# Kernel optimization log

Hardware: AMD Instinct MI355X
Metric: run time of the kernel (lower is better)

## Reference

```python
import jax, jax.numpy as jnp
import numpy as np

DEPTH = 2
NW = 4          # number of wires (qubits), fixed by 2x2 patches
NP = 14 * 14    # patches per image
NUM_CLASSES = 10


def _ry(theta):
    c = jnp.cos(theta / 2).astype(jnp.complex64)
    s = jnp.sin(theta / 2).astype(jnp.complex64)
    return jnp.stack([jnp.stack([c, -s], -1), jnp.stack([s, c], -1)], -2)


def _rx(theta):
    c = jnp.cos(theta / 2).astype(jnp.complex64)
    s = (-1j) * jnp.sin(theta / 2).astype(jnp.complex64)
    return jnp.stack([jnp.stack([c, s], -1), jnp.stack([s, c], -1)], -2)


def _rz(theta):
    em = jnp.exp(-0.5j * theta.astype(jnp.complex64))
    ep = jnp.exp(0.5j * theta.astype(jnp.complex64))
    z = jnp.zeros_like(em)
    return jnp.stack([jnp.stack([em, z], -1), jnp.stack([z, ep], -1)], -2)


def _apply1(state, mat, wire):
    # state: (N,2,2,2,2); mat: (2,2) shared or (N,2,2) per-patch
    s = jnp.moveaxis(state, 1 + wire, -1)
    if mat.ndim == 2:
        s = jnp.einsum('...i,ji->...j', s, mat)
    else:
        s = jnp.einsum('n...i,nji->n...j', s, mat)
    return jnp.moveaxis(s, -1, 1 + wire)


def _cnot(state, c, t):
    a0 = jnp.take(state, 0, axis=1 + c)
    a1 = jnp.take(state, 1, axis=1 + c)
    t_ax = 1 + t - (1 if t > c else 0)   # target axis index after control removed
    a1 = jnp.flip(a1, axis=t_ax)
    return jnp.stack([a0, a1], axis=1 + c)


def _circuit(angles, params):
    # angles: (N,4) RY-encoded patch pixels; params: (DEPTH,NW,3)
    N = angles.shape[0]
    state = jnp.zeros((N, 16), jnp.complex64).at[:, 0].set(1.0).reshape(N, 2, 2, 2, 2)
    for w in range(NW):
        state = _apply1(state, _ry(angles[:, w]), w)
    for d in range(DEPTH):
        for w in range(NW):
            state = _apply1(state, _rx(params[d, w, 0]), w)
            state = _apply1(state, _ry(params[d, w, 1]), w)
            state = _apply1(state, _rz(params[d, w, 2]), w)
        for w in range(NW - 1):
            state = _cnot(state, w, w + 1)
        state = _cnot(state, NW - 1, 0)
    probs = state.real ** 2 + state.imag ** 2   # (N,2,2,2,2)
    feats = []
    for w in range(NW):
        p = jnp.moveaxis(probs, 1 + w, 1).reshape(N, 2, 8)
        feats.append(p[:, 0].sum(-1) - p[:, 1].sum(-1))  # <Z_w>
    return jnp.stack(feats, -1)                  # (N,4)


def setup_inputs() -> dict:
    key = jax.random.key(0)
    k1, k2, k3 = jax.random.split(key, 3)
    B = 4096
    x = jax.random.uniform(k1, (B, 1, 28, 28), jnp.float32)
    params = jax.random.normal(k2, (DEPTH, NW, 3), jnp.float32)
    W = jax.random.normal(k3, (NUM_CLASSES, NW * NP), jnp.float32) * 0.02
    b = jnp.zeros((NUM_CLASSES,), jnp.float32)
    return {"x": x, "params": params, "W": W, "b": b}


def reference(x, params, W, b):
    B = x.shape[0]
    # extract all 196 2x2 patches, row-major within each patch (matches view(bsz,-1))
    patches = x[:, 0].reshape(B, 14, 2, 14, 2).transpose(0, 1, 3, 2, 4).reshape(B * NP, 4)
    feats = _circuit(patches, params).reshape(B, NP * NW)  # (B,784)
    logits = feats @ W.T + b
    return jax.nn.log_softmax(logits, axis=-1)
```

## Files before the change

### kernel.cpp

```cpp
#include <hip/hip_runtime.h>
#include <hip/hip_bf16.h>

#define NPATCH 196

__global__ __launch_bounds__(256) void quanv_setup(const float* __restrict__ P,
                                                   float* __restrict__ C) {
  __shared__ float Sr[2][16][16], Si[2][16][16];
  __shared__ float gc[24], gs[24];
  __shared__ float A[4][16][16];
  __shared__ float B0[4][3][8][8];
  __shared__ float B1[4][3][3][4][4];
  __shared__ float B2[4][3][3][3][2][2];
  const int tid = threadIdx.x;
  const int row = tid >> 4, col = tid & 15;

  if (tid < 24) {
    float s, c;
    __sincosf(0.5f * P[tid], &s, &c);
    gc[tid] = c; gs[tid] = s;
  }
  Sr[0][row][col] = (row == col) ? 1.0f : 0.0f;
  Si[0][row][col] = 0.0f;
  __syncthreads();

  int cur = 0;
  for (int d = 0; d < 2; ++d) {
    for (int w = 0; w < 4; ++w) {
      const int m = 8 >> w;
      const int par = row ^ m;
      for (int g = 0; g < 3; ++g) {
        const int gi = (d * 4 + w) * 3 + g;
        const float c = gc[gi], s = gs[gi];
        const float r0 = Sr[cur][row][col], i0 = Si[cur][row][col];
        const float r1 = Sr[cur][par][col], i1 = Si[cur][par][col];
        float rn, in_;
        if (g == 0) {
          rn = c * r0 + s * i1;
          in_ = c * i0 - s * r1;
        } else if (g == 1) {
          const float sg = (row & m) ? s : -s;
          rn = c * r0 + sg * r1;
          in_ = c * i0 + sg * i1;
        } else {
          const float sg = (row & m) ? s : -s;
          rn = c * r0 - sg * i0;
          in_ = c * i0 + sg * r0;
        }
        Sr[cur ^ 1][row][col] = rn;
        Si[cur ^ 1][row][col] = in_;
        cur ^= 1;
        __syncthreads();
      }
    }
    int k = row;
    k ^= (k & 1) ? 8 : 0;
    k ^= (k & 2) ? 1 : 0;
    k ^= (k & 4) ? 2 : 0;
    k ^= (k & 8) ? 4 : 0;
    const float pr = Sr[cur][k][col], pi = Si[cur][k][col];
    Sr[cur ^ 1][row][col] = pr;
    Si[cur ^ 1][row][col] = pi;
    cur ^= 1;
    __syncthreads();
  }

  {
    const int i = row, j = col;
    float s0 = 0, s1 = 0, s2 = 0, s3 = 0;
#pragma unroll
    for (int k = 0; k < 16; ++k) {
      const float pr = Sr[cur][k][i] * Sr[cur][k][j] + Si[cur][k][i] * Si[cur][k][j];
      s0 += (k & 8) ? -pr : pr;
      s1 += (k & 4) ? -pr : pr;
      s2 += (k & 2) ? -pr : pr;
      s3 += (k & 1) ? -pr : pr;
    }
    A[0][i][j] = s0; A[1][i][j] = s1; A[2][i][j] = s2; A[3][i][j] = s3;
  }
  __syncthreads();

  {
    const int w = tid >> 6, ip = (tid >> 3) & 7, jp = tid & 7;
    const float a00 = A[w][ip][jp],     a11 = A[w][ip + 8][jp + 8];
    const float a01 = A[w][ip][jp + 8], a10 = A[w][ip + 8][jp];
    B0[w][0][ip][jp] = 0.5f * (a00 + a11);
    B0[w][1][ip][jp] = 0.5f * (a00 - a11);
    B0[w][2][ip][jp] = 0.5f * (a01 + a10);
  }
  __syncthreads();
  if (tid < 192) {
    const int w = tid / 48, a0 = (tid / 16) % 3, ii = (tid >> 2) & 3, jj = tid & 3;
    const float a00 = B0[w][a0][ii][jj],     a11 = B0[w][a0][ii + 4][jj + 4];
    const float a01 = B0[w][a0][ii][jj + 4], a10 = B0[w][a0][ii + 4][jj];
    B1[w][a0][0][ii][jj] = 0.5f * (a00 + a11);
    B1[w][a0][1][ii][jj] = 0.5f * (a00 - a11);
    B1[w][a0][2][ii][jj] = 0.5f * (a01 + a10);
  }
  __syncthreads();
  if (tid < 144) {
    const int w = tid / 36, a0 = (tid / 12) % 3, a1 = (tid / 4) % 3;
    const int i3 = (tid >> 1) & 1, j3 = tid & 1;
    const float a00 = B1[w][a0][a1][i3][j3],     a11 = B1[w][a0][a1][i3 + 2][j3 + 2];
    const float a01 = B1[w][a0][a1][i3][j3 + 2], a10 = B1[w][a0][a1][i3 + 2][j3];
    B2[w][a0][a1][0][i3][j3] = 0.5f * (a00 + a11);
    B2[w][a0][a1][1][i3][j3] = 0.5f * (a00 - a11);
    B2[w][a0][a1][2][i3][j3] = 0.5f * (a01 + a10);
  }
  __syncthreads();
  if (tid < 108) {
    const int w = tid / 27, r = tid % 27;
    const int a0 = r / 9, a1 = (r / 3) % 3, a2 = r % 3;
    const float a00 = B2[w][a0][a1][a2][0][0], a11 = B2[w][a0][a1][a2][1][1];
    const float a01 = B2[w][a0][a1][a2][0][1], a10 = B2[w][a0][a1][a2][1][0];
    const int base = (3 * a0 + a1) * 9 + 3 * a2;
    C[(base + 0) * 4 + w] = 0.5f * (a00 + a11);
    C[(base + 1) * 4 + w] = 0.5f * (a00 - a11);
    C[(base + 2) * 4 + w] = 0.5f * (a01 + a10);
  }
}

__global__ __launch_bounds__(256) void quanv_main(const float* __restrict__ x,
                                                  const float* __restrict__ W,
                                                  const float* __restrict__ bias,
                                                  const float* __restrict__ C,
                                                  float* __restrict__ out) {
  __shared__ float wred[4][10];
  __shared__ float logits[10];
  __shared__ float snorm;
  const int tid = threadIdx.x;
  const int b = blockIdx.x;

  float lg[10];
#pragma unroll
  for (int k = 0; k < 10; ++k) lg[k] = 0.0f;

  if (tid < NPATCH) {
    const int pi = tid / 14, pj = tid - pi * 14;
    const float* px = x + b * 784 + pi * 56 + pj * 2;
    const float2 r0 = *reinterpret_cast<const float2*>(px);
    const float2 r1 = *reinterpret_cast<const float2*>(px + 28);
    float c0, s0, c1, s1, c2, s2, c3, s3;
    __sincosf(r0.x, &s0, &c0);
    __sincosf(r0.y, &s1, &c1);
    __sincosf(r1.x, &s2, &c2);
    __sincosf(r1.y, &s3, &c3);
    float m01[9], m23[9];
    m01[0] = 1.0f; m01[1] = c1;      m01[2] = s1;
    m01[3] = c0;   m01[4] = c0 * c1; m01[5] = c0 * s1;
    m01[6] = s0;   m01[7] = s0 * c1; m01[8] = s0 * s1;
    m23[0] = 1.0f; m23[1] = c3;      m23[2] = s3;
    m23[3] = c2;   m23[4] = c2 * c3; m23[5] = c2 * s3;
    m23[6] = s2;   m23[7] = s2 * c3; m23[8] = s2 * s3;

    float f0 = 0, f1 = 0, f2 = 0, f3 = 0;
    const float4* C4 = reinterpret_cast<const float4*>(C);
#pragma unroll
    for (int a = 0; a < 9; ++a) {
#pragma unroll
      for (int q = 0; q < 9; ++q) {
        const float pr = m01[a] * m23[q];
        const float4 cc = C4[a * 9 + q];
        f0 += cc.x * pr; f1 += cc.y * pr; f2 += cc.z * pr; f3 += cc.w * pr;
      }
    }
    const float* Wp = W + tid * 4;
#pragma unroll
    for (int k = 0; k < 10; ++k) {
      const float4 wv = *reinterpret_cast<const float4*>(Wp + k * 784);
      lg[k] = f0 * wv.x + f1 * wv.y + f2 * wv.z + f3 * wv.w;
    }
  }

#pragma unroll
  for (int k = 0; k < 10; ++k) {
    float v = lg[k];
    v += __shfl_xor(v, 32);
    v += __shfl_xor(v, 16);
    v += __shfl_xor(v, 8);
    v += __shfl_xor(v, 4);
    v += __shfl_xor(v, 2);
    v += __shfl_xor(v, 1);
    lg[k] = v;
  }
  const int lane = tid & 63, wid = tid >> 6;
  if (lane == 0) {
#pragma unroll
    for (int k = 0; k < 10; ++k) wred[wid][k] = lg[k];
  }
  __syncthreads();
  if (tid < 10)
    logits[tid] = wred[0][tid] + wred[1][tid] + wred[2][tid] + wred[3][tid] + bias[tid];
  __syncthreads();
  if (tid == 0) {
    float m = logits[0];
#pragma unroll
    for (int k = 1; k < 10; ++k) m = fmaxf(m, logits[k]);
    float se = 0;
#pragma unroll
    for (int k = 0; k < 10; ++k) se += expf(logits[k] - m);
    snorm = m + logf(se);
  }
  __syncthreads();
  if (tid < 10) out[b * 10 + tid] = logits[tid] - snorm;
}

extern "C" void kernel_launch(void* const* d_in, const int* in_sizes, int n_in,
                              void* d_out, int out_size, void* d_ws, size_t ws_size,
                              hipStream_t stream) {
  const float* x = (const float*)d_in[0];
  const float* P = (const float*)d_in[1];
  const float* W = (const float*)d_in[2];
  const float* bias = (const float*)d_in[3];
  float* out = (float*)d_out;
  float* C = (float*)d_ws;
  const int B = out_size / 10;

  quanv_setup<<<1, 256, 0, stream>>>(P, C);
  quanv_main<<<B, 256, 0, stream>>>(x, W, bias, C, out);
}
```

Before: 27.60 us.

## Fuse rotation gates into unitaries, pack FMAs, restructure logit reduction

In the setup kernel, each wire's RX·RY·RZ gates are combined into one precomputed 2x2 complex unitary, so 24 gate steps become 8 and there are fewer barriers. The final CNOT permutation is no longer a separate pass; it is folded into the index used by the expectation-matrix build. In the main kernel, the 81-term contraction is factorized into an inner sum over q and an outer scale by a, using two-wide float vectors so the compiler can emit packed FMAs. The wave-wide shuffle reduction is replaced by a 4-lane shuffle plus a 49-entry shared-memory sum done serially by 10 threads, which may add latency to the block tail.

```diff
diff --git a/kernel.cpp b/kernel.cpp
--- a/kernel.cpp
+++ b/kernel.cpp
@@ -3,10 +3,13 @@
 
 #define NPATCH 196
 
+typedef float f2 __attribute__((ext_vector_type(2)));
+
 __global__ __launch_bounds__(256) void quanv_setup(const float* __restrict__ P,
                                                    float* __restrict__ C) {
+  __shared__ float gc[24], gs[24];
+  __shared__ float Ur[8][2][2], Ui[8][2][2];
   __shared__ float Sr[2][16][16], Si[2][16][16];
-  __shared__ float gc[24], gs[24];
   __shared__ float A[4][16][16];
   __shared__ float B0[4][3][8][8];
   __shared__ float B1[4][3][3][4][4];
@@ -23,45 +26,53 @@
   Si[0][row][col] = 0.0f;
   __syncthreads();
 
+  if (tid < 8) {
+    const int base = tid * 3;
+    const float c1 = gc[base], s1 = gs[base];
+    const float c2 = gc[base + 1], s2 = gs[base + 1];
+    const float c3 = gc[base + 2], s3 = gs[base + 2];
+    const float m00r = c2 * c1, m00i = s2 * s1;
+    const float m01r = -s2 * c1, m01i = -c2 * s1;
+    const float m10r = s2 * c1, m10i = -c2 * s1;
+    const float m11r = c2 * c1, m11i = -s2 * s1;
+    Ur[tid][0][0] = c3 * m00r + s3 * m00i;  Ui[tid][0][0] = c3 * m00i - s3 * m00r;
+    Ur[tid][0][1] = c3 * m01r + s3 * m01i;  Ui[tid][0][1] = c3 * m01i - s3 * m01r;
+    Ur[tid][1][0] = c3 * m10r - s3 * m10i;  Ui[tid][1][0] = c3 * m10i + s3 * m10r;
+    Ur[tid][1][1] = c3 * m11r - s3 * m11i;  Ui[tid][1][1] = c3 * m11i + s3 * m11r;
+  }
+  __syncthreads();
+
   int cur = 0;
   for (int d = 0; d < 2; ++d) {
     for (int w = 0; w < 4; ++w) {
+      const int gi = d * 4 + w;
       const int m = 8 >> w;
+      const int bit = (row & m) ? 1 : 0;
       const int par = row ^ m;
-      for (int g = 0; g < 3; ++g) {
-        const int gi = (d * 4 + w) * 3 + g;
-        const float c = gc[gi], s = gs[gi];
-        const float r0 = Sr[cur][row][col], i0 = Si[cur][row][col];
-        const float r1 = Sr[cur][par][col], i1 = Si[cur][par][col];
-        float rn, in_;
-        if (g == 0) {
-          rn = c * r0 + s * i1;
-          in_ = c * i0 - s * r1;
-        } else if (g == 1) {
-          const float sg = (row & m) ? s : -s;
-          rn = c * r0 + sg * r1;
-          in_ = c * i0 + sg * i1;
-        } else {
-          const float sg = (row & m) ? s : -s;
-          rn = c * r0 - sg * i0;
-          in_ = c * i0 + sg * r0;
-        }
-        Sr[cur ^ 1][row][col] = rn;
-        Si[cur ^ 1][row][col] = in_;
-        cur ^= 1;
-        __syncthreads();
-      }
-    }
-    int k = row;
-    k ^= (k & 1) ? 8 : 0;
-    k ^= (k & 2) ? 1 : 0;
-    k ^= (k & 4) ? 2 : 0;
-    k ^= (k & 8) ? 4 : 0;
-    const float pr = Sr[cur][k][col], pi = Si[cur][k][col];
-    Sr[cur ^ 1][row][col] = pr;
-    Si[cur ^ 1][row][col] = pi;
-    cur ^= 1;
-    __syncthreads();
+      const int r0 = bit ? par : row, r1 = bit ? row : par;
+      const float a_r = Sr[cur][r0][col], a_i = Si[cur][r0][col];
+      const float b_r = Sr[cur][r1][col], b_i = Si[cur][r1][col];
+      const float u0r = Ur[gi][bit][0], u0i = Ui[gi][bit][0];
+      const float u1r = Ur[gi][bit][1], u1i = Ui[gi][bit][1];
+      const float rn = u0r * a_r - u0i * a_i + u1r * b_r - u1i * b_i;
+      const float in_ = u0r * a_i + u0i * a_r + u1r * b_i + u1i * b_r;
+      Sr[cur ^ 1][row][col] = rn;
+      Si[cur ^ 1][row][col] = in_;
+      cur ^= 1;
+      __syncthreads();
+    }
+    if (d == 0) {
+      int k = row;
+      k ^= (k & 1) ? 8 : 0;
+      k ^= (k & 2) ? 1 : 0;
+      k ^= (k & 4) ? 2 : 0;
+      k ^= (k & 8) ? 4 : 0;
+      const float pr_ = Sr[cur][k][col], pi_ = Si[cur][k][col];
+      Sr[cur ^ 1][row][col] = pr_;
+      Si[cur ^ 1][row][col] = pi_;
+      cur ^= 1;
+      __syncthreads();
+    }
   }
 
   {
@@ -69,7 +80,12 @@
     float s0 = 0, s1 = 0, s2 = 0, s3 = 0;
 #pragma unroll
     for (int k = 0; k < 16; ++k) {
-      const float pr = Sr[cur][k][i] * Sr[cur][k][j] + Si[cur][k][i] * Si[cur][k][j];
+      int gk = k;
+      gk ^= (gk & 1) ? 8 : 0;
+      gk ^= (gk & 2) ? 1 : 0;
+      gk ^= (gk & 4) ? 2 : 0;
+      gk ^= (gk & 8) ? 4 : 0;
+      const float pr = Sr[cur][gk][i] * Sr[cur][gk][j] + Si[cur][gk][i] * Si[cur][gk][j];
       s0 += (k & 8) ? -pr : pr;
       s1 += (k & 4) ? -pr : pr;
       s2 += (k & 2) ? -pr : pr;
@@ -124,7 +140,7 @@
                                                   const float* __restrict__ bias,
                                                   const float* __restrict__ C,
                                                   float* __restrict__ out) {
-  __shared__ float wred[4][10];
+  __shared__ float red2[49][10];
   __shared__ float logits[10];
   __shared__ float snorm;
   const int tid = threadIdx.x;
@@ -144,52 +160,53 @@
     __sincosf(r0.y, &s1, &c1);
     __sincosf(r1.x, &s2, &c2);
     __sincosf(r1.y, &s3, &c3);
-    float m01[9], m23[9];
-    m01[0] = 1.0f; m01[1] = c1;      m01[2] = s1;
-    m01[3] = c0;   m01[4] = c0 * c1; m01[5] = c0 * s1;
-    m01[6] = s0;   m01[7] = s0 * c1; m01[8] = s0 * s1;
-    m23[0] = 1.0f; m23[1] = c3;      m23[2] = s3;
-    m23[3] = c2;   m23[4] = c2 * c3; m23[5] = c2 * s3;
-    m23[6] = s2;   m23[7] = s2 * c3; m23[8] = s2 * s3;
-
-    float f0 = 0, f1 = 0, f2 = 0, f3 = 0;
-    const float4* C4 = reinterpret_cast<const float4*>(C);
+    const float m01s[9] = {1.0f, c1, s1, c0, c0 * c1, c0 * s1, s0, s0 * c1, s0 * s1};
+    const float m23s[9] = {1.0f, c3, s3, c2, c2 * c3, c2 * s3, s2, s2 * c3, s2 * s3};
+    f2 m23b[9];
+#pragma unroll
+    for (int q = 0; q < 9; ++q) m23b[q] = (f2){m23s[q], m23s[q]};
+
+    f2 f01 = {0.0f, 0.0f}, f23 = {0.0f, 0.0f};
+    const f2* C2 = reinterpret_cast<const f2*>(C);
 #pragma unroll
     for (int a = 0; a < 9; ++a) {
+      f2 t01 = {0.0f, 0.0f}, t23 = {0.0f, 0.0f};
 #pragma unroll
       for (int q = 0; q < 9; ++q) {
-        const float pr = m01[a] * m23[q];
-        const float4 cc = C4[a * 9 + q];
-        f0 += cc.x * pr; f1 += cc.y * pr; f2 += cc.z * pr; f3 += cc.w * pr;
+        const int idx = (a * 9 + q) * 2;
+        t01 += C2[idx] * m23b[q];
+        t23 += C2[idx + 1] * m23b[q];
       }
-    }
+      f01 += t01 * m01s[a];
+      f23 += t23 * m01s[a];
+    }
+    const float f0 = f01.x, f1 = f01.y, f2v = f23.x, f3 = f23.y;
+
     const float* Wp = W + tid * 4;
 #pragma unroll
     for (int k = 0; k < 10; ++k) {
       const float4 wv = *reinterpret_cast<const float4*>(Wp + k * 784);
-      lg[k] = f0 * wv.x + f1 * wv.y + f2 * wv.z + f3 * wv.w;
+      lg[k] = f0 * wv.x + f1 * wv.y + f2v * wv.z + f3 * wv.w;
     }
   }
 
 #pragma unroll
   for (int k = 0; k < 10; ++k) {
-    float v = lg[k];
-    v += __shfl_xor(v, 32);
-    v += __shfl_xor(v, 16);
-    v += __shfl_xor(v, 8);
-    v += __shfl_xor(v, 4);
-    v += __shfl_xor(v, 2);
-    v += __shfl_xor(v, 1);
-    lg[k] = v;
-  }
-  const int lane = tid & 63, wid = tid >> 6;
-  if (lane == 0) {
-#pragma unroll
-    for (int k = 0; k < 10; ++k) wred[wid][k] = lg[k];
-  }
-  __syncthreads();
-  if (tid < 10)
-    logits[tid] = wred[0][tid] + wred[1][tid] + wred[2][tid] + wred[3][tid] + bias[tid];
+    lg[k] += __shfl_xor(lg[k], 1);
+    lg[k] += __shfl_xor(lg[k], 2);
+  }
+  if (tid < NPATCH) {
+    const int g = tid >> 2, sub = tid & 3;
+#pragma unroll
+    for (int k = 0; k < 10; ++k)
+      if ((k & 3) == sub) red2[g][k] = lg[k];
+  }
+  __syncthreads();
+  if (tid < 10) {
+    float s = bias[tid];
+    for (int g2 = 0; g2 < 49; ++g2) s += red2[g2][tid];
+    logits[tid] = s;
+  }
   __syncthreads();
   if (tid == 0) {
     float m = logits[0];
```

After: 24.43 us. 1.13x faster.
